# Optimization experiments

Hardware: AMD Instinct MI355X
Metric: run time of the kernel (lower is better)

## Reference

```python
import jax, jax.numpy as jnp
import numpy as np

B, T, S, C = 16, 2048, 512, 192
NEG = -1e9  # large-negative stand-in for float32.min (avoids overflow when accumulated)


def setup_inputs() -> dict:
    key = jax.random.key(0)
    ks = jax.random.split(key, 6)
    m_p = jax.random.normal(ks[0], (B, S, C), jnp.float32)
    logs_p = jax.random.normal(ks[1], (B, S, C), jnp.float32) * 0.1
    z_p = jax.random.normal(ks[2], (B, T, C), jnp.float32)
    logs_q = jax.random.normal(ks[3], (B, T, C), jnp.float32) * 0.1
    textlen = jax.random.randint(ks[4], (B,), S // 2, S + 1, jnp.int32)
    mellen = jax.random.randint(ks[5], (B,), T // 2, T + 1, jnp.int32)
    return dict(m_p=m_p, logs_p=logs_p, z_p=z_p, logs_q=logs_q,
                textlen=textlen, mellen=mellen)


def monotonic_alignment_search(ll, textlen, mellen):
    """Viterbi-style monotonic alignment. ll: [B, T, S] -> attn [B, T, S]."""
    Bb, Tt, Ss = ll.shape
    s_range = jnp.arange(Ss)
    ll_t = jnp.transpose(ll, (1, 0, 2))  # [T, B, S]

    def fwd(prob, xt):
        t, ll_row = xt
        prev = jnp.concatenate([jnp.full((Bb, 1), NEG, ll.dtype), prob[:, :-1]], axis=1)
        stay = prob >= prev  # True: best path stays at same text index
        prob = jnp.where(s_range[None] <= t, jnp.maximum(prob, prev) + ll_row, NEG)
        return prob, stay

    _, direction = jax.lax.scan(fwd, jnp.zeros((Bb, Ss), ll.dtype),
                                (jnp.arange(Tt), ll_t))  # direction: [T, B, S] bool

    def bwd(idx, xt):
        t, dir_t = xt
        active = t < mellen  # [B]
        onehot = (s_range[None] == idx[:, None]) & active[:, None]  # [B, S]
        stay = jnp.take_along_axis(dir_t, idx[:, None], axis=1)[:, 0]
        new_idx = jnp.where(active, idx - (1 - stay.astype(jnp.int32)), idx)
        return new_idx, onehot

    _, attn_rev = jax.lax.scan(bwd, textlen - 1,
                               (jnp.arange(Tt - 1, -1, -1), direction[::-1]))
    attn = attn_rev[::-1].astype(ll.dtype)  # [T, B, S]
    return jnp.transpose(attn, (1, 0, 2))


def reference(m_p, logs_p, z_p, logs_q, textlen, mellen):
    tmask = (jnp.arange(S)[None] < textlen[:, None]).astype(jnp.float32)  # [B, S]
    mmask = (jnp.arange(T)[None] < mellen[:, None]).astype(jnp.float32)   # [B, T]
    attnmask = mmask[:, :, None] * tmask[:, None]                          # [B, T, S]

    # Negative cross-entropy score matrix [B, T, S]
    s_sq_r = jnp.exp(-2.0 * logs_p)  # [B, S, C]
    nc1 = jnp.sum(-0.5 * np.log(2.0 * np.pi) - logs_p, axis=-1)[:, None]  # [B, 1, S]
    nc2 = jnp.einsum('btc,bsc->bts', -0.5 * z_p ** 2, s_sq_r)
    nc3 = jnp.einsum('btc,bsc->bts', z_p, m_p * s_sq_r)
    nc4 = jnp.sum(-0.5 * m_p ** 2 * s_sq_r, axis=-1)[:, None]             # [B, 1, S]
    neg_cent = nc1 + nc2 + nc3 + nc4

    ll = jnp.where(attnmask > 0, neg_cent, NEG)
    attn = jax.lax.stop_gradient(monotonic_alignment_search(ll, textlen, mellen))

    # Expand text-level stats to frame level via the hard alignment
    m_e = jnp.einsum('bts,bsc->btc', attn, m_p)
    l_e = jnp.einsum('bts,bsc->btc', attn, logs_p)

    kl = l_e - logs_q - 0.5 + 0.5 * (z_p - m_e) ** 2 * jnp.exp(-2.0 * l_e)
    kl = jnp.sum(kl * mmask[..., None]) / jnp.sum(mmask)
    return kl, attn
```

## Files before the change

kernel.cpp:

```cpp
#include <hip/hip_runtime.h>
#include <hip/hip_fp16.h>

#define NEGV (-1e9f)

static const int B_ = 16;
static const int T_ = 2048;
static const int S_ = 512;
static const int C_ = 192;

typedef unsigned short ushort_t;
using f32x4 = __attribute__((ext_vector_type(4))) float;
using s16x8 = __attribute__((ext_vector_type(8))) short;

__device__ __forceinline__ void split2(float x, ushort_t& h, ushort_t& l) {
    __bf16 hb = (__bf16)x;
    h = __builtin_bit_cast(ushort_t, hb);
    float r = x - (float)hb;
    __bf16 lb = (__bf16)r;
    l = __builtin_bit_cast(ushort_t, lb);
}

__global__ __launch_bounds__(256)
void prep_kernel(const float* __restrict__ m_p, const float* __restrict__ logs_p,
                 ushort_t* __restrict__ Bh, ushort_t* __restrict__ Bl,
                 float* __restrict__ nc14) {
    int wid = (blockIdx.x * blockDim.x + threadIdx.x) >> 6;
    int lane = threadIdx.x & 63;
    if (wid >= B_ * S_) return;
    const float HALF_LOG_2PI = 0.9189385332046727f;
    const float* mrow = m_p    + (size_t)wid * C_;
    const float* lrow = logs_p + (size_t)wid * C_;
    ushort_t* bh = Bh + (size_t)wid * 384;
    ushort_t* bl = Bl + (size_t)wid * 384;
    float tot = 0.f;
#pragma unroll
    for (int q = 0; q < 3; ++q) {
        int c = lane + q * 64;
        float m  = mrow[c];
        float lp = lrow[c];
        float s2r = __expf(-2.f * lp);
        float a = m * s2r;
        ushort_t h, l;
        split2(a, h, l);   bh[c] = h;        bl[c] = l;
        split2(s2r, h, l); bh[192 + c] = h;  bl[192 + c] = l;
        tot += (-HALF_LOG_2PI - lp) + (-0.5f * m * m * s2r);
    }
#pragma unroll
    for (int off = 32; off > 0; off >>= 1) tot += __shfl_xor(tot, off);
    if (lane == 0) nc14[wid] = tot;
}

#define LDP 40
__global__ __launch_bounds__(256)
void gemm_kernel(const float* __restrict__ z_p,
                 const ushort_t* __restrict__ Bh, const ushort_t* __restrict__ Bl,
                 const float* __restrict__ nc14,
                 const int* __restrict__ textlen, const int* __restrict__ mellen,
                 __half* __restrict__ ll16) {
    __shared__ ushort_t sAh[128 * LDP];
    __shared__ ushort_t sAl[128 * LDP];
    __shared__ ushort_t sBh[128 * LDP];
    __shared__ ushort_t sBl[128 * LDP];

    const int b  = blockIdx.z;
    const int t0 = blockIdx.y * 128;
    const int s0 = blockIdx.x * 128;
    const int tid = threadIdx.x;
    const int lane = tid & 63;
    const int wave = tid >> 6;
    const int wr = wave >> 1, wc = wave & 1;
    const int srow = tid >> 1;
    const int cb = (tid & 1) * 16;

    f32x4 acc[4][4];
#pragma unroll
    for (int m = 0; m < 4; ++m)
#pragma unroll
        for (int n = 0; n < 4; ++n) acc[m][n] = (f32x4){0.f, 0.f, 0.f, 0.f};

    const int r15 = lane & 15;
    const int klane = (lane >> 4) * 8;

    for (int kk = 0; kk < 12; ++kk) {
        {
            const int ck = (kk < 6 ? kk * 32 : (kk - 6) * 32) + cb;
            const float* src = z_p + ((size_t)b * T_ + t0 + srow) * C_ + ck;
            float e[16];
            *(float4*)(e + 0)  = *(const float4*)(src + 0);
            *(float4*)(e + 4)  = *(const float4*)(src + 4);
            *(float4*)(e + 8)  = *(const float4*)(src + 8);
            *(float4*)(e + 12) = *(const float4*)(src + 12);
            if (kk >= 6) {
#pragma unroll
                for (int i = 0; i < 16; ++i) e[i] = -0.5f * e[i] * e[i];
            }
            ushort_t h[16], l[16];
#pragma unroll
            for (int i = 0; i < 16; ++i) split2(e[i], h[i], l[i]);
            ushort_t* dh = &sAh[srow * LDP + cb];
            ushort_t* dl = &sAl[srow * LDP + cb];
            *(uint4*)dh = make_uint4(h[0] | (h[1] << 16), h[2] | (h[3] << 16),
                                     h[4] | (h[5] << 16), h[6] | (h[7] << 16));
            *(uint4*)(dh + 8) = make_uint4(h[8] | (h[9] << 16), h[10] | (h[11] << 16),
                                           h[12] | (h[13] << 16), h[14] | (h[15] << 16));
            *(uint4*)dl = make_uint4(l[0] | (l[1] << 16), l[2] | (l[3] << 16),
                                     l[4] | (l[5] << 16), l[6] | (l[7] << 16));
            *(uint4*)(dl + 8) = make_uint4(l[8] | (l[9] << 16), l[10] | (l[11] << 16),
                                           l[12] | (l[13] << 16), l[14] | (l[15] << 16));
        }
        {
            const size_t off = ((size_t)b * S_ + s0 + srow) * 384 + kk * 32 + cb;
            const uint4 u0 = *(const uint4*)(Bh + off);
            const uint4 u1 = *(const uint4*)(Bh + off + 8);
            const uint4 v0 = *(const uint4*)(Bl + off);
            const uint4 v1 = *(const uint4*)(Bl + off + 8);
            ushort_t* dh = &sBh[srow * LDP + cb];
            ushort_t* dl = &sBl[srow * LDP + cb];
            *(uint4*)dh = u0; *(uint4*)(dh + 8) = u1;
            *(uint4*)dl = v0; *(uint4*)(dl + 8) = v1;
        }
        __syncthreads();

        s16x8 ah[4], al[4], bhf[4], blf[4];
#pragma unroll
        for (int m = 0; m < 4; ++m) {
            const int row = wr * 64 + m * 16 + r15;
            ah[m] = *(const s16x8*)&sAh[row * LDP + klane];
            al[m] = *(const s16x8*)&sAl[row * LDP + klane];
        }
#pragma unroll
        for (int n = 0; n < 4; ++n) {
            const int row = wc * 64 + n * 16 + r15;
            bhf[n] = *(const s16x8*)&sBh[row * LDP + klane];
            blf[n] = *(const s16x8*)&sBl[row * LDP + klane];
        }
#pragma unroll
        for (int m = 0; m < 4; ++m)
#pragma unroll
            for (int n = 0; n < 4; ++n) {
                acc[m][n] = __builtin_amdgcn_mfma_f32_16x16x32_bf16(ah[m], bhf[n], acc[m][n], 0, 0, 0);
                acc[m][n] = __builtin_amdgcn_mfma_f32_16x16x32_bf16(ah[m], blf[n], acc[m][n], 0, 0, 0);
                acc[m][n] = __builtin_amdgcn_mfma_f32_16x16x32_bf16(al[m], bhf[n], acc[m][n], 0, 0, 0);
            }
        __syncthreads();
    }

    const int ml = mellen[b], tl = textlen[b];
    int scol[4]; float ncv[4];
#pragma unroll
    for (int n = 0; n < 4; ++n) {
        scol[n] = s0 + wc * 64 + n * 16 + r15;
        ncv[n] = nc14[b * S_ + scol[n]];
    }
#pragma unroll
    for (int m = 0; m < 4; ++m) {
        const int tb = t0 + wr * 64 + m * 16 + (lane >> 4) * 4;
#pragma unroll
        for (int r = 0; r < 4; ++r) {
            const int t = tb + r;
            const bool tm = (t < ml);
            __half* orow = ll16 + ((size_t)b * T_ + t) * S_;
#pragma unroll
            for (int n = 0; n < 4; ++n)
                orow[scol[n]] = __float2half(
                    (tm && scol[n] < tl) ? (acc[m][n][r] + ncv[n]) : NEGV);
        }
    }
}

#define RINGH 8
__global__ __launch_bounds__(64)
void mas_forward(const __half* __restrict__ ll16, unsigned char* __restrict__ dir) {
    const int b = blockIdx.x;
    const int lane = threadIdx.x;
    const __half* llb = ll16 + (size_t)b * T_ * S_ + lane * 8;
    unsigned char* db = dir + ((size_t)b * T_) * 64 + lane;
    const int sbase = lane * 8;

    uint2 pre[RINGH][2];
#pragma unroll
    for (int r = 0; r < RINGH; ++r) {
        pre[r][0] = *(const uint2*)(llb + (size_t)r * S_);
        pre[r][1] = *(const uint2*)(llb + (size_t)r * S_ + 4);
    }

    float p[8];
#pragma unroll
    for (int j = 0; j < 8; ++j) p[j] = 0.f;
    float carry = (lane == 0) ? NEGV : 0.f;

    auto step = [&](int t, int ph, bool masked) {
        uint2 u0 = pre[ph][0];
        uint2 u1 = pre[ph][1];
        const int tn = t + RINGH;
        if (tn < T_) {
            pre[ph][0] = *(const uint2*)(llb + (size_t)tn * S_);
            pre[ph][1] = *(const uint2*)(llb + (size_t)tn * S_ + 4);
        }
        float2 f0 = __half22float2(__builtin_bit_cast(__half2, u0.x));
        float2 f1 = __half22float2(__builtin_bit_cast(__half2, u0.y));
        float2 f2 = __half22float2(__builtin_bit_cast(__half2, u1.x));
        float2 f3 = __half22float2(__builtin_bit_cast(__half2, u1.y));
        float cur[8];
        cur[0] = f0.x; cur[1] = f0.y; cur[2] = f1.x; cur[3] = f1.y;
        cur[4] = f2.x; cur[5] = f2.y; cur[6] = f3.x; cur[7] = f3.y;

        float v7 = fmaxf(p[7], p[6]) + cur[7];
        float nc7 = masked ? ((sbase + 7 <= t) ? v7 : NEGV) : v7;
        float newcarry = __shfl_up(nc7, 1);

        unsigned bits = (p[0] >= carry) ? 1u : 0u;
#pragma unroll
        for (int j = 1; j < 8; ++j)
            bits |= (p[j] >= p[j - 1] ? 1u : 0u) << j;

        float nv[8];
        nv[0] = fmaxf(p[0], carry) + cur[0];
#pragma unroll
        for (int j = 1; j < 7; ++j) nv[j] = fmaxf(p[j], p[j - 1]) + cur[j];
        nv[7] = v7;
        if (masked) {
#pragma unroll
            for (int j = 0; j < 8; ++j)
                p[j] = (sbase + j <= t) ? nv[j] : NEGV;
        } else {
#pragma unroll
            for (int j = 0; j < 8; ++j) p[j] = nv[j];
        }
        carry = (lane == 0) ? NEGV : newcarry;
        db[(size_t)t * 64] = (unsigned char)bits;
    };

    for (int to = 0; to < S_ / 8; ++to) {
#pragma unroll
        for (int ph = 0; ph < 8; ++ph) step(to * 8 + ph, ph, true);
    }
    for (int to = S_ / 8; to < T_ / 8; ++to) {
#pragma unroll
        for (int ph = 0; ph < 8; ++ph) step(to * 8 + ph, ph, false);
    }
}

__global__ __launch_bounds__(64)
void mas_backward(const unsigned char* __restrict__ dir,
                  const int* __restrict__ textlen, const int* __restrict__ mellen,
                  int* __restrict__ idx_arr) {
    const int b = blockIdx.x;
    const int lane = threadIdx.x;
    const int tl = textlen[b], ml = mellen[b];
    for (int t = ml + lane; t < T_; t += 64) idx_arr[b * T_ + t] = -1;
    const unsigned char* db = dir + (size_t)b * T_ * 64;
    int idx = tl - 1;
    int t_hi = ml - 1;
    while (t_hi >= 0) {
        const int lo = idx - 7;
        const int blo = (lo > 0 ? lo : 0) >> 3;
        const int bhi = idx >> 3;
        const int t = t_hi - lane;
        unsigned v = 0;
        if (lane < 8 && t >= 0) {
            unsigned b0 = db[(size_t)t * 64 + blo];
            unsigned b1 = db[(size_t)t * 64 + bhi];
            v = b0 | (b1 << 8);
        }
        unsigned vk[8];
#pragma unroll
        for (int k = 0; k < 8; ++k) vk[k] = __shfl((int)v, k);
        int emit = -1;
#pragma unroll
        for (int k = 0; k < 8; ++k) {
            const int tt = t_hi - k;
            if (tt < 0) break;
            if (lane == k) emit = idx;
            const int sb = idx >> 3;
            const unsigned byte = (sb == bhi) ? (vk[k] >> 8) : (vk[k] & 0xffu);
            const int stay = (byte >> (idx & 7)) & 1;
            idx -= (1 - stay);
            if (idx < 0) idx = 0;
        }
        const int tt = t_hi - lane;
        if (lane < 8 && tt >= 0) idx_arr[b * T_ + tt] = emit;
        t_hi -= 8;
    }
}

__global__ __launch_bounds__(256)
void scatter_attn(const int* __restrict__ idx_arr, float* __restrict__ attn) {
    const int f = blockIdx.x * blockDim.x + threadIdx.x;
    if (f >= B_ * T_) return;
    const int idx = idx_arr[f];
    if (idx >= 0) attn[(size_t)f * S_ + idx] = 1.0f;
}

__global__ __launch_bounds__(256)
void kl_frames(const float* __restrict__ m_p, const float* __restrict__ logs_p,
               const float* __restrict__ z_p, const float* __restrict__ logs_q,
               const int* __restrict__ idx_arr, const int* __restrict__ mellen,
               float* __restrict__ frame_kl) {
    const int wid = (blockIdx.x * blockDim.x + threadIdx.x) >> 6;
    const int lane = threadIdx.x & 63;
    if (wid >= B_ * T_) return;
    const int b = wid >> 11;
    const int t = wid & (T_ - 1);
    const int ml = mellen[b];
    float total = 0.f;
    if (t < ml) {
        const int idx = idx_arr[wid];
        const float* mr = m_p    + ((size_t)b * S_ + idx) * C_;
        const float* lr = logs_p + ((size_t)b * S_ + idx) * C_;
        const float* zr = z_p    + (size_t)wid * C_;
        const float* qr = logs_q + (size_t)wid * C_;
#pragma unroll
        for (int q = 0; q < 3; ++q) {
            const int c = lane + q * 64;
            const float le = lr[c];
            const float d = zr[c] - mr[c];
            total += le - qr[c] - 0.5f + 0.5f * d * d * __expf(-2.f * le);
        }
    }
#pragma unroll
    for (int off = 32; off > 0; off >>= 1) total += __shfl_xor(total, off);
    if (lane == 0) frame_kl[wid] = total;
}

__global__ __launch_bounds__(256)
void kl_reduce(const float* __restrict__ frame_kl, const int* __restrict__ mellen,
               float* __restrict__ out) {
    __shared__ float sm[256];
    const int tid = threadIdx.x;
    float s = 0.f;
    for (int k = tid; k < B_ * T_; k += 256) s += frame_kl[k];
    sm[tid] = s;
    __syncthreads();
    for (int off = 128; off > 0; off >>= 1) {
        if (tid < off) sm[tid] += sm[tid + off];
        __syncthreads();
    }
    if (tid == 0) {
        int sum_ml = 0;
        for (int bq = 0; bq < B_; ++bq) sum_ml += mellen[bq];
        out[0] = sm[0] / (float)sum_ml;
    }
}

extern "C" void kernel_launch(void* const* d_in, const int* in_sizes, int n_in,
                              void* d_out, int out_size, void* d_ws, size_t ws_size,
                              hipStream_t stream) {
    const float* m_p    = (const float*)d_in[0];
    const float* logs_p = (const float*)d_in[1];
    const float* z_p    = (const float*)d_in[2];
    const float* logs_q = (const float*)d_in[3];
    const int*   textlen = (const int*)d_in[4];
    const int*   mellen  = (const int*)d_in[5];

    float* out = (float*)d_out;
    float* attn = out + 1;
    __half* ll16 = (__half*)((char*)d_out + 16);

    char* ws = (char*)d_ws;
    const size_t OFF_BH   = 0;
    const size_t OFF_BL   = OFF_BH + (size_t)B_ * S_ * 384 * 2;
    const size_t OFF_NC   = OFF_BL + (size_t)B_ * S_ * 384 * 2;
    const size_t OFF_DIR  = OFF_NC + (size_t)B_ * S_ * 4;
    const size_t OFF_IDX  = OFF_DIR + (size_t)B_ * T_ * 64;
    const size_t OFF_FKL  = OFF_IDX + (size_t)B_ * T_ * 4;
    ushort_t* Bh = (ushort_t*)(ws + OFF_BH);
    ushort_t* Bl = (ushort_t*)(ws + OFF_BL);
    float* nc14 = (float*)(ws + OFF_NC);
    unsigned char* dir = (unsigned char*)(ws + OFF_DIR);
    int* idx_arr = (int*)(ws + OFF_IDX);
    float* frame_kl = (float*)(ws + OFF_FKL);

    prep_kernel<<<(B_ * S_) / 4, 256, 0, stream>>>(m_p, logs_p, Bh, Bl, nc14);
    gemm_kernel<<<dim3(S_ / 128, T_ / 128, B_), 256, 0, stream>>>(
        z_p, Bh, Bl, nc14, textlen, mellen, ll16);
    mas_forward<<<B_, 64, 0, stream>>>(ll16, dir);
    mas_backward<<<B_, 64, 0, stream>>>(dir, textlen, mellen, idx_arr);
    hipMemsetAsync(attn, 0, (size_t)B_ * T_ * S_ * 4, stream);
    scatter_attn<<<(B_ * T_ + 255) / 256, 256, 0, stream>>>(idx_arr, attn);
    kl_frames<<<(B_ * T_) / 4, 256, 0, stream>>>(m_p, logs_p, z_p, logs_q,
                                                 idx_arr, mellen, frame_kl);
    kl_reduce<<<1, 256, 0, stream>>>(frame_kl, mellen, out);
}
```

Measured before the change: 526.9 us.

## Process two batch rows per wavefront in MAS forward for ILP

The MAS forward kernel now runs two independent batch rows in one 64-lane wavefront, interleaving their Viterbi recurrences. It launches 8 blocks instead of 16 and loads each row's fp16 slice with one 16-byte load instead of two 8-byte loads. The aim is to hide the latency of the serial per-timestep dependency chain (shuffle, max, add) by overlapping two independent chains in one wave. The cost is fewer waves, so fewer CUs are in use, and higher register pressure from the doubled prefetch ring and state.

New measurement: 1.586 ms. 3.01x slower.

```diff
diff --git a/kernel.cpp b/kernel.cpp
--- a/kernel.cpp
+++ b/kernel.cpp
@@ -171,36 +171,33 @@
 #define RINGH 8
 __global__ __launch_bounds__(64)
 void mas_forward(const __half* __restrict__ ll16, unsigned char* __restrict__ dir) {
-    const int b = blockIdx.x;
+    const int bb = blockIdx.x;
     const int lane = threadIdx.x;
-    const __half* llb = ll16 + (size_t)b * T_ * S_ + lane * 8;
-    unsigned char* db = dir + ((size_t)b * T_) * 64 + lane;
+    const __half* llb0 = ll16 + (size_t)(2 * bb) * T_ * S_ + lane * 8;
+    const __half* llb1 = llb0 + (size_t)T_ * S_;
+    unsigned char* db0 = dir + (size_t)(2 * bb) * T_ * 64 + lane;
+    unsigned char* db1 = db0 + (size_t)T_ * 64;
     const int sbase = lane * 8;
 
-    uint2 pre[RINGH][2];
+    uint4 pre0[RINGH], pre1[RINGH];
 #pragma unroll
     for (int r = 0; r < RINGH; ++r) {
-        pre[r][0] = *(const uint2*)(llb + (size_t)r * S_);
-        pre[r][1] = *(const uint2*)(llb + (size_t)r * S_ + 4);
-    }
-
-    float p[8];
-#pragma unroll
-    for (int j = 0; j < 8; ++j) p[j] = 0.f;
-    float carry = (lane == 0) ? NEGV : 0.f;
-
-    auto step = [&](int t, int ph, bool masked) {
-        uint2 u0 = pre[ph][0];
-        uint2 u1 = pre[ph][1];
-        const int tn = t + RINGH;
-        if (tn < T_) {
-            pre[ph][0] = *(const uint2*)(llb + (size_t)tn * S_);
-            pre[ph][1] = *(const uint2*)(llb + (size_t)tn * S_ + 4);
-        }
-        float2 f0 = __half22float2(__builtin_bit_cast(__half2, u0.x));
-        float2 f1 = __half22float2(__builtin_bit_cast(__half2, u0.y));
-        float2 f2 = __half22float2(__builtin_bit_cast(__half2, u1.x));
-        float2 f3 = __half22float2(__builtin_bit_cast(__half2, u1.y));
+        pre0[r] = *(const uint4*)(llb0 + (size_t)r * S_);
+        pre1[r] = *(const uint4*)(llb1 + (size_t)r * S_);
+    }
+
+    float p0[8], p1[8];
+#pragma unroll
+    for (int j = 0; j < 8; ++j) { p0[j] = 0.f; p1[j] = 0.f; }
+    float carry0 = (lane == 0) ? NEGV : 0.f;
+    float carry1 = carry0;
+
+    auto half_step = [&](uint4 u, float* p, float& carry, int t,
+                         bool masked) -> unsigned {
+        float2 f0 = __half22float2(__builtin_bit_cast(__half2, u.x));
+        float2 f1 = __half22float2(__builtin_bit_cast(__half2, u.y));
+        float2 f2 = __half22float2(__builtin_bit_cast(__half2, u.z));
+        float2 f3 = __half22float2(__builtin_bit_cast(__half2, u.w));
         float cur[8];
         cur[0] = f0.x; cur[1] = f0.y; cur[2] = f1.x; cur[3] = f1.y;
         cur[4] = f2.x; cur[5] = f2.y; cur[6] = f3.x; cur[7] = f3.y;
@@ -228,7 +225,21 @@
             for (int j = 0; j < 8; ++j) p[j] = nv[j];
         }
         carry = (lane == 0) ? NEGV : newcarry;
-        db[(size_t)t * 64] = (unsigned char)bits;
+        return bits;
+    };
+
+    auto step = [&](int t, int ph, bool masked) {
+        uint4 u0 = pre0[ph];
+        uint4 u1 = pre1[ph];
+        const int tn = t + RINGH;
+        if (tn < T_) {
+            pre0[ph] = *(const uint4*)(llb0 + (size_t)tn * S_);
+            pre1[ph] = *(const uint4*)(llb1 + (size_t)tn * S_);
+        }
+        unsigned bits0 = half_step(u0, p0, carry0, t, masked);
+        unsigned bits1 = half_step(u1, p1, carry1, t, masked);
+        db0[(size_t)t * 64] = (unsigned char)bits0;
+        db1[(size_t)t * 64] = (unsigned char)bits1;
     };
 
     for (int to = 0; to < S_ / 8; ++to) {
@@ -374,7 +385,7 @@
     prep_kernel<<<(B_ * S_) / 4, 256, 0, stream>>>(m_p, logs_p, Bh, Bl, nc14);
     gemm_kernel<<<dim3(S_ / 128, T_ / 128, B_), 256, 0, stream>>>(
         z_p, Bh, Bl, nc14, textlen, mellen, ll16);
-    mas_forward<<<B_, 64, 0, stream>>>(ll16, dir);
+    mas_forward<<<B_ / 2, 64, 0, stream>>>(ll16, dir);
     mas_backward<<<B_, 64, 0, stream>>>(dir, textlen, mellen, idx_arr);
     hipMemsetAsync(attn, 0, (size_t)B_ * T_ * S_ * 4, stream);
     scatter_attn<<<(B_ * T_ + 255) / 256, 256, 0, stream>>>(idx_arr, attn);
```
